# Performance work log

Hardware: AMD Instinct MI355X
Metric: run time of the kernel (lower is better)

## Reference

```python
import jax, jax.numpy as jnp
import numpy as np

B, T, E, H = 512, 256, 384, 64

def setup_inputs() -> dict:
    key = jax.random.key(0)
    k1, k2, k3, k4 = jax.random.split(key, 4)
    scale = 1.0 / np.sqrt(E)
    return {
        "x":  jax.random.normal(k1, (B, T, E), dtype=jnp.float32),
        "Wq": jax.random.normal(k2, (E, H), dtype=jnp.float32) * scale,
        "Wk": jax.random.normal(k3, (E, H), dtype=jnp.float32) * scale,
        "Wv": jax.random.normal(k4, (E, H), dtype=jnp.float32) * scale,
    }

def reference(x, Wq, Wk, Wv):
    # single-head causal self-attention (dropout in eval mode / identity)
    q = jnp.einsum('bte,eh->bth', x, Wq)
    k = jnp.einsum('bte,eh->bth', x, Wk)
    v = jnp.einsum('bte,eh->bth', x, Wv)
    d = q.shape[-1]
    wei = jnp.einsum('bqh,bkh->bqk', q, k) * (d ** -0.5)   # [B,T,T]
    T_ = x.shape[1]
    causal = jnp.tril(jnp.ones((T_, T_), dtype=bool))
    wei = jnp.where(causal[None, :, :], wei, -jnp.inf)
    wei = jax.nn.softmax(wei, axis=-1)
    out = jnp.einsum('bqk,bkh->bqh', wei, v)               # [B,T,H]
    return out
```

## Files before the change

kernel.cpp:

```cpp
#include <hip/hip_runtime.h>

typedef __attribute__((ext_vector_type(4)))  float f32x4;
typedef __attribute__((ext_vector_type(16))) float f32x16;
typedef __attribute__((ext_vector_type(8)))  short s16x8;
typedef __attribute__((ext_vector_type(4)))  short s16x4;


__device__ inline short f2bf(float f){
  unsigned u = __float_as_uint(f);
  u = u + 0x7fffu + ((u >> 16) & 1u);
  return (short)(u >> 16);
}

__device__ __forceinline__ void gld16(const void* g, void* l){
  __builtin_amdgcn_global_load_lds((const __attribute__((address_space(1))) void*)g,
                                   (__attribute__((address_space(3))) void*)l, 16, 0, 0);
}

__global__ void wt_prep_kernel(const float* __restrict__ Wq, const float* __restrict__ Wk,
                               const float* __restrict__ Wv, short* __restrict__ Wt){
  int o = blockIdx.x * 256 + threadIdx.x;
  if (o >= 192*384) return;
  int n = o / 384, k = o - n*384;
  const float* W = (n < 64) ? Wq : (n < 128) ? Wk : Wv;
  Wt[o] = f2bf(W[k*64 + (n & 63)]);
}

__global__ __launch_bounds__(512, 4) void qkv_kernel(const float* __restrict__ x,
    const short* __restrict__ Wt, short* __restrict__ Qg,
    short* __restrict__ Kg, short* __restrict__ Vg){
  const int tid  = threadIdx.x;
  const int w    = tid >> 6, lane = tid & 63;
  const int l15  = lane & 15, quad = lane >> 4;
  const int b    = blockIdx.x;

  const float* xb = x + (long)b*256*384;
  short* Qb = Qg + (long)b*16384;
  char*  Kb = (char*)(Kg + (long)b*16384);
  char*  Vb = (char*)(Vg + (long)b*16384);

  #pragma unroll 1
  for (int p = 0; p < 2; ++p){
    const int r0 = w*32 + p*16;
    const int tr = r0 + l15;

    f32x4 aq[4], ak[4], av[4];
    #pragma unroll
    for (int c = 0; c < 4; ++c)
      #pragma unroll
      for (int i = 0; i < 4; ++i){ aq[c][i]=0.f; ak[c][i]=0.f; av[c][i]=0.f; }

    const float* xr = xb + (long)tr*384;
    #pragma unroll 2
    for (int kt = 0; kt < 12; ++kt){
      const int k0 = kt*32 + quad*8;
      float4 a0 = *(const float4*)(xr + k0);
      float4 a1 = *(const float4*)(xr + k0 + 4);
      s16x8 bx;
      bx[0]=f2bf(a0.x); bx[1]=f2bf(a0.y); bx[2]=f2bf(a0.z); bx[3]=f2bf(a0.w);
      bx[4]=f2bf(a1.x); bx[5]=f2bf(a1.y); bx[6]=f2bf(a1.z); bx[7]=f2bf(a1.w);
      #pragma unroll
      for (int c = 0; c < 4; ++c){
        s16x8 wq = *(const s16x8*)(Wt + (c*16 + l15)*384 + k0);
        aq[c] = __builtin_amdgcn_mfma_f32_16x16x32_bf16(wq, bx, aq[c], 0, 0, 0);
      }
      #pragma unroll
      for (int c = 0; c < 4; ++c){
        s16x8 wk = *(const s16x8*)(Wt + ((c+4)*16 + l15)*384 + k0);
        ak[c] = __builtin_amdgcn_mfma_f32_16x16x32_bf16(wk, bx, ak[c], 0, 0, 0);
      }
      #pragma unroll
      for (int c = 0; c < 4; ++c){
        s16x8 wv = *(const s16x8*)(Wt + ((c+8)*16 + l15)*384 + k0);
        av[c] = __builtin_amdgcn_mfma_f32_16x16x32_bf16(bx, wv, av[c], 0, 0, 0);
      }
    }

    #pragma unroll
    for (int c = 0; c < 4; ++c){
      s16x4 v;
      #pragma unroll
      for (int i = 0; i < 4; ++i) v[i] = f2bf(aq[c][i]);
      *(s16x4*)(Qb + tr*64 + c*16 + quad*4) = v;
    }
    {
      const int swz = (tr & 7) << 4;
      #pragma unroll
      for (int c = 0; c < 4; ++c){
        s16x4 v;
        #pragma unroll
        for (int i = 0; i < 4; ++i) v[i] = f2bf(ak[c][i]);
        *(s16x4*)(Kb + tr*128 + ((c*32 + quad*8) ^ swz)) = v;
      }
    }
    #pragma unroll
    for (int c = 0; c < 4; ++c){
      const int h   = c*16 + l15;
      const int swz = (h & 7) << 4;
      s16x4 v;
      #pragma unroll
      for (int i = 0; i < 4; ++i) v[i] = f2bf(av[c][i]);
      *(s16x4*)(Vb + h*512 + (((r0 + quad*4)*2) ^ swz)) = v;
    }
  }
}

__global__ __launch_bounds__(512, 4) void attn_kernel(const short* __restrict__ Qg,
    const short* __restrict__ Kg, const short* __restrict__ Vg,
    float* __restrict__ out){
  __shared__ __align__(16) short Ks[16384];
  __shared__ __align__(16) short Vts[16384];
  __shared__ __align__(16) short Pp[8][16*40];

  const int tid  = threadIdx.x;
  const int w    = tid >> 6, lane = tid & 63;
  const int l15  = lane & 15, quad = lane >> 4;
  const int b    = blockIdx.x;

  const short* Qb = Qg + (long)b*16384;
  const int F0 = w, F1 = 15 - w;
  s16x8 qA0 = *(const s16x8*)(Qb + (F0*16 + l15)*64 + quad*8);
  s16x8 qA1 = *(const s16x8*)(Qb + (F0*16 + l15)*64 + 32 + quad*8);
  s16x8 qB0 = *(const s16x8*)(Qb + (F1*16 + l15)*64 + quad*8);
  s16x8 qB1 = *(const s16x8*)(Qb + (F1*16 + l15)*64 + 32 + quad*8);

  const char* Kb = (const char*)(Kg + (long)b*16384);
  const char* Vb = (const char*)(Vg + (long)b*16384);
  {
    const int base = w*4096;
    #pragma unroll
    for (int i = 0; i < 4; ++i){
      gld16(Kb + base + i*1024 + lane*16, (char*)Ks  + base + i*1024);
      gld16(Vb + base + i*1024 + lane*16, (char*)Vts + base + i*1024);
    }
  }
  __syncthreads();

  float* ob = out + (long)b*256*64;
  short* Pw = Pp[w];
  const int swz = (l15 & 7) << 4;

  auto attend = [&](int F, s16x8 qf0, s16x8 qf1){
    const int qb = F*16;
    const int NF = F + 1;
    const int NS = (NF + 1) >> 1;

    f32x4 sc[16];
    #pragma unroll
    for (int f = 0; f < 16; ++f){
      f32x4 a;
      #pragma unroll
      for (int r = 0; r < 4; ++r) a[r] = 0.0f;
      if (f < NF){
        const char* kp = (const char*)Ks + (f*16 + l15)*128;
        s16x8 k0v = *(const s16x8*)(kp + ((quad*16)      ^ swz));
        s16x8 k1v = *(const s16x8*)(kp + ((64 + quad*16) ^ swz));
        a = __builtin_amdgcn_mfma_f32_16x16x32_bf16(qf0, k0v, a, 0, 0, 0);
        a = __builtin_amdgcn_mfma_f32_16x16x32_bf16(qf1, k1v, a, 0, 0, 0);
      }
      sc[f] = a;
    }

    float mx[4], sm[4];
    #pragma unroll
    for (int r = 0; r < 4; ++r) mx[r] = -3.0e38f;
    #pragma unroll
    for (int f = 0; f < 16; ++f){
      if (f < NF){
        const int key = f*16 + l15;
        #pragma unroll
        for (int r = 0; r < 4; ++r){
          const int qg = qb + quad*4 + r;
          float s = sc[f][r] * 0.125f;
          s = (key <= qg) ? s : -1.0e30f;
          sc[f][r] = s;
          mx[r] = fmaxf(mx[r], s);
        }
      }
    }
    #pragma unroll
    for (int r = 0; r < 4; ++r){
      #pragma unroll
      for (int off = 1; off < 16; off <<= 1) mx[r] = fmaxf(mx[r], __shfl_xor(mx[r], off, 16));
    }
    #pragma unroll
    for (int r = 0; r < 4; ++r) sm[r] = 0.0f;
    #pragma unroll
    for (int f = 0; f < 16; ++f){
      if (f < NF){
        #pragma unroll
        for (int r = 0; r < 4; ++r){
          float p = exp2f((sc[f][r] - mx[r]) * 1.44269504f);
          sc[f][r] = p;
          sm[r] += p;
        }
      }
    }
    #pragma unroll
    for (int r = 0; r < 4; ++r){
      #pragma unroll
      for (int off = 1; off < 16; off <<= 1) sm[r] += __shfl_xor(sm[r], off, 16);
    }

    f32x4 o[4];
    #pragma unroll
    for (int h0 = 0; h0 < 4; ++h0)
      #pragma unroll
      for (int r = 0; r < 4; ++r) o[h0][r] = 0.0f;

    #pragma unroll
    for (int ks = 0; ks < 8; ++ks){
      if (ks < NS){
        #pragma unroll
        for (int fi = 0; fi < 2; ++fi){
          const int f = 2*ks + fi;
          #pragma unroll
          for (int r = 0; r < 4; ++r){
            short v = 0;
            if (f < NF) v = f2bf(sc[f][r]);
            Pw[(quad*4 + r)*40 + fi*16 + l15] = v;
          }
        }
        s16x8 pf = *(const s16x8*)(Pw + l15*40 + quad*8);
        #pragma unroll
        for (int h0 = 0; h0 < 4; ++h0){
          const char* vp = (const char*)Vts + (h0*16 + l15)*512;
          s16x8 vf = *(const s16x8*)(vp + ((ks*64 + quad*16) ^ swz));
          o[h0] = __builtin_amdgcn_mfma_f32_16x16x32_bf16(pf, vf, o[h0], 0, 0, 0);
        }
      }
    }

    #pragma unroll
    for (int r = 0; r < 4; ++r){
      const float inv = 1.0f / sm[r];
      #pragma unroll
      for (int h0 = 0; h0 < 4; ++h0)
        ob[(qb + quad*4 + r)*64 + h0*16 + l15] = o[h0][r] * inv;
    }
  };
  attend(F0, qA0, qA1);
  attend(F1, qB0, qB1);
}

__global__ __launch_bounds__(512, 2) void fused_kernel(const float* __restrict__ x,
                             const short* __restrict__ Wt, float* __restrict__ out){
  __shared__ __align__(16) short Qs[256*72];
  __shared__ __align__(16) short Ks2[256*72];
  __shared__ __align__(16) short Vts2[64*264];
  __shared__ __align__(16) short Pp2[8][16*40];

  const int tid  = threadIdx.x;
  const int w    = tid >> 6, lane = tid & 63;
  const int l31  = lane & 31, hh = lane >> 5;
  const int b    = blockIdx.x;

  const float* xb = x + ((long)b*256 + w*32)*384;

  f32x16 acc[6];
  #pragma unroll
  for (int c = 0; c < 6; ++c)
    #pragma unroll
    for (int j = 0; j < 16; ++j) acc[c][j] = 0.0f;

  #pragma unroll 2
  for (int kt = 0; kt < 6; ++kt){
    #pragma unroll
    for (int s = 0; s < 4; ++s){
      const int k0 = kt*64 + s*16 + hh*8;
      const float* xp = xb + l31*384 + k0;
      float4 a0 = *(const float4*)xp;
      float4 a1 = *(const float4*)(xp + 4);
      s16x8 bx;
      bx[0]=f2bf(a0.x); bx[1]=f2bf(a0.y); bx[2]=f2bf(a0.z); bx[3]=f2bf(a0.w);
      bx[4]=f2bf(a1.x); bx[5]=f2bf(a1.y); bx[6]=f2bf(a1.z); bx[7]=f2bf(a1.w);
      #pragma unroll
      for (int c = 0; c < 6; ++c){
        s16x8 wa = *(const s16x8*)(Wt + (c*32 + l31)*384 + k0);
        acc[c] = __builtin_amdgcn_mfma_f32_32x32x16_bf16(wa, bx, acc[c], 0, 0, 0);
      }
    }
  }

  const int trow = w*32 + l31;
  #pragma unroll
  for (int c = 0; c < 4; ++c){
    short* dst = (c < 2) ? Qs : Ks2;
    const int nb = (c & 1)*32;
    #pragma unroll
    for (int g = 0; g < 4; ++g){
      s16x4 v;
      #pragma unroll
      for (int i = 0; i < 4; ++i) v[i] = f2bf(acc[c][g*4 + i]);
      *(s16x4*)(dst + trow*72 + nb + 8*g + 4*hh) = v;
    }
  }
  #pragma unroll
  for (int c = 4; c < 6; ++c)
    #pragma unroll
    for (int reg = 0; reg < 16; ++reg){
      const int h = (c-4)*32 + (reg & 3) + 8*(reg >> 2) + 4*hh;
      Vts2[h*264 + trow] = f2bf(acc[c][reg]);
    }

  __syncthreads();

  const int l15 = lane & 15, quad = lane >> 4;
  float* ob = out + (long)b*256*64;
  short* Pw = Pp2[w];

  for (int it = 0; it < 2; ++it){
    const int F  = it ? (15 - w) : w;
    const int qb = F*16;
    const int NF = F + 1;
    const int NS = (NF + 1) >> 1;

    s16x8 qf0 = *(const s16x8*)(Qs + (qb + l15)*72 + quad*8);
    s16x8 qf1 = *(const s16x8*)(Qs + (qb + l15)*72 + 32 + quad*8);

    f32x4 sc[16];
    #pragma unroll
    for (int f = 0; f < 16; ++f){
      f32x4 a;
      #pragma unroll
      for (int r = 0; r < 4; ++r) a[r] = 0.0f;
      if (f < NF){
        const short* kp = Ks2 + (f*16 + l15)*72 + quad*8;
        s16x8 k0v = *(const s16x8*)kp;
        s16x8 k1v = *(const s16x8*)(kp + 32);
        a = __builtin_amdgcn_mfma_f32_16x16x32_bf16(qf0, k0v, a, 0, 0, 0);
        a = __builtin_amdgcn_mfma_f32_16x16x32_bf16(qf1, k1v, a, 0, 0, 0);
      }
      sc[f] = a;
    }

    float mx[4], sm[4];
    #pragma unroll
    for (int r = 0; r < 4; ++r) mx[r] = -3.0e38f;
    #pragma unroll
    for (int f = 0; f < 16; ++f){
      if (f < NF){
        const int key = f*16 + l15;
        #pragma unroll
        for (int r = 0; r < 4; ++r){
          const int qg = qb + quad*4 + r;
          float s = sc[f][r] * 0.125f;
          s = (key <= qg) ? s : -1.0e30f;
          sc[f][r] = s;
          mx[r] = fmaxf(mx[r], s);
        }
      }
    }
    #pragma unroll
    for (int r = 0; r < 4; ++r){
      #pragma unroll
      for (int off = 1; off < 16; off <<= 1) mx[r] = fmaxf(mx[r], __shfl_xor(mx[r], off, 16));
    }
    #pragma unroll
    for (int r = 0; r < 4; ++r) sm[r] = 0.0f;
    #pragma unroll
    for (int f = 0; f < 16; ++f){
      if (f < NF){
        #pragma unroll
        for (int r = 0; r < 4; ++r){
          float p = exp2f((sc[f][r] - mx[r]) * 1.44269504f);
          sc[f][r] = p;
          sm[r] += p;
        }
      }
    }
    #pragma unroll
    for (int r = 0; r < 4; ++r){
      #pragma unroll
      for (int off = 1; off < 16; off <<= 1) sm[r] += __shfl_xor(sm[r], off, 16);
    }

    f32x4 o[4];
    #pragma unroll
    for (int h0 = 0; h0 < 4; ++h0)
      #pragma unroll
      for (int r = 0; r < 4; ++r) o[h0][r] = 0.0f;

    #pragma unroll
    for (int ks = 0; ks < 8; ++ks){
      if (ks < NS){
        #pragma unroll
        for (int fi = 0; fi < 2; ++fi){
          const int f = 2*ks + fi;
          #pragma unroll
          for (int r = 0; r < 4; ++r){
            short v = 0;
            if (f < NF) v = f2bf(sc[f][r]);
            Pw[(quad*4 + r)*40 + fi*16 + l15] = v;
          }
        }
        s16x8 pf = *(const s16x8*)(Pw + l15*40 + quad*8);
        #pragma unroll
        for (int h0 = 0; h0 < 4; ++h0){
          s16x8 vf = *(const s16x8*)(Vts2 + (h0*16 + l15)*264 + ks*32 + quad*8);
          o[h0] = __builtin_amdgcn_mfma_f32_16x16x32_bf16(pf, vf, o[h0], 0, 0, 0);
        }
      }
    }

    #pragma unroll
    for (int r = 0; r < 4; ++r){
      const float inv = 1.0f / sm[r];
      #pragma unroll
      for (int h0 = 0; h0 < 4; ++h0)
        ob[(qb + quad*4 + r)*64 + h0*16 + l15] = o[h0][r] * inv;
    }
  }
}

extern "C" void kernel_launch(void* const* d_in, const int* in_sizes, int n_in,
                              void* d_out, int out_size, void* d_ws, size_t ws_size,
                              hipStream_t stream){
  const float* x  = (const float*)d_in[0];
  const float* Wq = (const float*)d_in[1];
  const float* Wk = (const float*)d_in[2];
  const float* Wv = (const float*)d_in[3];
  float* out = (float*)d_out;

  short* Wt = (short*)d_ws;
  const size_t need = 147456 + 3ull*16777216ull;

  hipLaunchKernelGGL(wt_prep_kernel, dim3(288), dim3(256), 0, stream, Wq, Wk, Wv, Wt);
  if (ws_size >= need){
    short* Qg = (short*)((char*)d_ws + 147456);
    short* Kg = Qg + 8388608;
    short* Vg = Kg + 8388608;
    hipLaunchKernelGGL(qkv_kernel,  dim3(512), dim3(512), 0, stream, x, Wt, Qg, Kg, Vg);
    hipLaunchKernelGGL(attn_kernel, dim3(512), dim3(512), 0, stream, Qg, Kg, Vg, out);
  } else {
    hipLaunchKernelGGL(fused_kernel, dim3(512), dim3(512), 0, stream, x, Wt, out);
  }
}
```

Baseline: 424.1 us.

## Restructure QKV projection with LDS-staged double-buffered x tiles and 32x32 MFMA

The QKV projection kernel now splits each batch across two blocks of 128 rows. It stages x tiles into swizzled LDS with async global-to-LDS loads, double-buffered across the K loop, and computes with 32x32x16 MFMAs split across two warp groups. This targets the strided, uncoalesced per-lane global reads of x and raises parallelism, at the cost of a barrier each K step. The fallback fused kernel is also replaced by one that projects into LDS directly with the attention tiling, but that path likely does not run when the workspace is large enough.

```diff
diff --git a/kernel.cpp b/kernel.cpp
--- a/kernel.cpp
+++ b/kernel.cpp
@@ -26,31 +26,283 @@
   Wt[o] = f2bf(W[k*64 + (n & 63)]);
 }
 
-__global__ __launch_bounds__(512, 4) void qkv_kernel(const float* __restrict__ x,
+__global__ __launch_bounds__(512, 4) void qkv2_kernel(const float* __restrict__ x,
     const short* __restrict__ Wt, short* __restrict__ Qg,
     short* __restrict__ Kg, short* __restrict__ Vg){
+  __shared__ __align__(16) float xs[2][128][32];
+
+  const int tid  = threadIdx.x;
+  const int w    = tid >> 6, lane = tid & 63;
+  const int l31  = lane & 31, hh = lane >> 5;
+  const int wn   = w >> 2,  wt = w & 3;
+  const int b    = blockIdx.x >> 1;
+  const int t0   = (blockIdx.x & 1) << 7;
+
+  const char* xbase = (const char*)x + ((long)b*256 + t0)*1536;
+
+  auto stage = [&](int kt, int buf){
+    #pragma unroll
+    for (int i2 = 0; i2 < 2; ++i2){
+      const int ii = w*2 + i2;
+      const int r  = ii*8 + (lane >> 3);
+      const char* src = xbase + (long)r*1536 + kt*128
+                      + ((((lane & 7) ^ (lane >> 3)) << 4));
+      gld16(src, (char*)&xs[buf][ii*8][0]);
+    }
+  };
+
+  f32x16 acc[3];
+  #pragma unroll
+  for (int c = 0; c < 3; ++c)
+    #pragma unroll
+    for (int i = 0; i < 16; ++i) acc[c][i] = 0.0f;
+
+  const int swr = (l31 & 7) << 4;
+  const short* wrow = Wt + (wn*96 + l31)*384;
+
+  stage(0, 0);
+  __syncthreads();
+
+  for (int kt = 0; kt < 12; ++kt){
+    if (kt < 11) stage(kt + 1, (kt + 1) & 1);
+
+    const char* bp = (const char*)&xs[kt & 1][wt*32 + l31][0];
+    #pragma unroll
+    for (int s = 0; s < 2; ++s){
+      const int c0 = s*64 + hh*32;
+      f32x4 a0 = *(const f32x4*)(bp + ((c0     ) ^ swr));
+      f32x4 a1 = *(const f32x4*)(bp + ((c0 + 16) ^ swr));
+      s16x8 bx;
+      bx[0]=f2bf(a0[0]); bx[1]=f2bf(a0[1]); bx[2]=f2bf(a0[2]); bx[3]=f2bf(a0[3]);
+      bx[4]=f2bf(a1[0]); bx[5]=f2bf(a1[1]); bx[6]=f2bf(a1[2]); bx[7]=f2bf(a1[3]);
+
+      const short* wp = wrow + kt*32 + s*16 + hh*8;
+      s16x8 w0 = *(const s16x8*)(wp);
+      s16x8 w1 = *(const s16x8*)(wp + 32*384);
+      s16x8 w2 = *(const s16x8*)(wp + 64*384);
+      if (wn == 0){
+        acc[0] = __builtin_amdgcn_mfma_f32_32x32x16_bf16(w0, bx, acc[0], 0, 0, 0);
+        acc[1] = __builtin_amdgcn_mfma_f32_32x32x16_bf16(w1, bx, acc[1], 0, 0, 0);
+        acc[2] = __builtin_amdgcn_mfma_f32_32x32x16_bf16(w2, bx, acc[2], 0, 0, 0);
+      } else {
+        acc[0] = __builtin_amdgcn_mfma_f32_32x32x16_bf16(w0, bx, acc[0], 0, 0, 0);
+        acc[1] = __builtin_amdgcn_mfma_f32_32x32x16_bf16(bx, w1, acc[1], 0, 0, 0);
+        acc[2] = __builtin_amdgcn_mfma_f32_32x32x16_bf16(bx, w2, acc[2], 0, 0, 0);
+      }
+    }
+    __syncthreads();
+  }
+
+  const int tl = t0 + wt*32 + l31;
+  short* Qb = Qg + (long)b*16384;
+  char*  Kb = (char*)(Kg + (long)b*16384);
+  char*  Vb = (char*)(Vg + (long)b*16384);
+
+  if (wn == 0){
+    #pragma unroll
+    for (int c = 0; c < 2; ++c)
+      #pragma unroll
+      for (int g = 0; g < 4; ++g){
+        s16x4 v;
+        #pragma unroll
+        for (int j = 0; j < 4; ++j) v[j] = f2bf(acc[c][4*g + j]);
+        *(s16x4*)(Qb + (long)tl*64 + c*32 + 8*g + 4*hh) = v;
+      }
+    const int swk = (tl & 7) << 4;
+    #pragma unroll
+    for (int g = 0; g < 4; ++g){
+      s16x4 v;
+      #pragma unroll
+      for (int j = 0; j < 4; ++j) v[j] = f2bf(acc[2][4*g + j]);
+      *(s16x4*)(Kb + (long)tl*128 + ((16*g + 8*hh) ^ swk)) = v;
+    }
+  } else {
+    const int swk = (tl & 7) << 4;
+    #pragma unroll
+    for (int g = 0; g < 4; ++g){
+      s16x4 v;
+      #pragma unroll
+      for (int j = 0; j < 4; ++j) v[j] = f2bf(acc[0][4*g + j]);
+      *(s16x4*)(Kb + (long)tl*128 + ((64 + 16*g + 8*hh) ^ swk)) = v;
+    }
+    #pragma unroll
+    for (int c = 1; c < 3; ++c){
+      const int h   = (c - 1)*32 + l31;
+      const int swv = (h & 7) << 4;
+      #pragma unroll
+      for (int g = 0; g < 4; ++g){
+        const int tb = t0 + wt*32 + 8*g + 4*hh;
+        s16x4 v;
+        #pragma unroll
+        for (int j = 0; j < 4; ++j) v[j] = f2bf(acc[c][4*g + j]);
+        *(s16x4*)(Vb + (long)h*512 + ((tb*2) ^ swv)) = v;
+      }
+    }
+  }
+}
+
+__global__ __launch_bounds__(512, 4) void attn_kernel(const short* __restrict__ Qg,
+    const short* __restrict__ Kg, const short* __restrict__ Vg,
+    float* __restrict__ out){
+  __shared__ __align__(16) short Ks[16384];
+  __shared__ __align__(16) short Vts[16384];
+  __shared__ __align__(16) short Pp[8][16*40];
+
   const int tid  = threadIdx.x;
   const int w    = tid >> 6, lane = tid & 63;
   const int l15  = lane & 15, quad = lane >> 4;
   const int b    = blockIdx.x;
 
+  const short* Qb = Qg + (long)b*16384;
+  const int F0 = w, F1 = 15 - w;
+  s16x8 qA0 = *(const s16x8*)(Qb + (F0*16 + l15)*64 + quad*8);
+  s16x8 qA1 = *(const s16x8*)(Qb + (F0*16 + l15)*64 + 32 + quad*8);
+  s16x8 qB0 = *(const s16x8*)(Qb + (F1*16 + l15)*64 + quad*8);
+  s16x8 qB1 = *(const s16x8*)(Qb + (F1*16 + l15)*64 + 32 + quad*8);
+
+  const char* Kb = (const char*)(Kg + (long)b*16384);
+  const char* Vb = (const char*)(Vg + (long)b*16384);
+  {
+    const int base = w*4096;
+    #pragma unroll
+    for (int i = 0; i < 4; ++i){
+      gld16(Kb + base + i*1024 + lane*16, (char*)Ks  + base + i*1024);
+      gld16(Vb + base + i*1024 + lane*16, (char*)Vts + base + i*1024);
+    }
+  }
+  __syncthreads();
+
+  float* ob = out + (long)b*256*64;
+  short* Pw = Pp[w];
+  const int swz = (l15 & 7) << 4;
+
+  auto attend = [&](int F, s16x8 qf0, s16x8 qf1){
+    const int qb = F*16;
+    const int NF = F + 1;
+    const int NS = (NF + 1) >> 1;
+
+    f32x4 sc[16];
+    #pragma unroll
+    for (int f = 0; f < 16; ++f){
+      f32x4 a;
+      #pragma unroll
+      for (int r = 0; r < 4; ++r) a[r] = 0.0f;
+      if (f < NF){
+        const char* kp = (const char*)Ks + (f*16 + l15)*128;
+        s16x8 k0v = *(const s16x8*)(kp + ((quad*16)      ^ swz));
+        s16x8 k1v = *(const s16x8*)(kp + ((64 + quad*16) ^ swz));
+        a = __builtin_amdgcn_mfma_f32_16x16x32_bf16(qf0, k0v, a, 0, 0, 0);
+        a = __builtin_amdgcn_mfma_f32_16x16x32_bf16(qf1, k1v, a, 0, 0, 0);
+      }
+      sc[f] = a;
+    }
+
+    float mx[4], sm[4];
+    #pragma unroll
+    for (int r = 0; r < 4; ++r) mx[r] = -3.0e38f;
+    #pragma unroll
+    for (int f = 0; f < 16; ++f){
+      if (f < NF){
+        const int key = f*16 + l15;
+        #pragma unroll
+        for (int r = 0; r < 4; ++r){
+          const int qg = qb + quad*4 + r;
+          float s = sc[f][r] * 0.125f;
+          s = (key <= qg) ? s : -1.0e30f;
+          sc[f][r] = s;
+          mx[r] = fmaxf(mx[r], s);
+        }
+      }
+    }
+    #pragma unroll
+    for (int r = 0; r < 4; ++r){
+      #pragma unroll
+      for (int off = 1; off < 16; off <<= 1) mx[r] = fmaxf(mx[r], __shfl_xor(mx[r], off, 16));
+    }
+    #pragma unroll
+    for (int r = 0; r < 4; ++r) sm[r] = 0.0f;
+    #pragma unroll
+    for (int f = 0; f < 16; ++f){
+      if (f < NF){
+        #pragma unroll
+        for (int r = 0; r < 4; ++r){
+          float p = exp2f((sc[f][r] - mx[r]) * 1.44269504f);
+          sc[f][r] = p;
+          sm[r] += p;
+        }
+      }
+    }
+    #pragma unroll
+    for (int r = 0; r < 4; ++r){
+      #pragma unroll
+      for (int off = 1; off < 16; off <<= 1) sm[r] += __shfl_xor(sm[r], off, 16);
+    }
+
+    f32x4 o[4];
+    #pragma unroll
+    for (int h0 = 0; h0 < 4; ++h0)
+      #pragma unroll
+      for (int r = 0; r < 4; ++r) o[h0][r] = 0.0f;
+
+    #pragma unroll
+    for (int ks = 0; ks < 8; ++ks){
+      if (ks < NS){
+        #pragma unroll
+        for (int fi = 0; fi < 2; ++fi){
+          const int f = 2*ks + fi;
+          #pragma unroll
+          for (int r = 0; r < 4; ++r){
+            short v = 0;
+            if (f < NF) v = f2bf(sc[f][r]);
+            Pw[(quad*4 + r)*40 + fi*16 + l15] = v;
+          }
+        }
+        s16x8 pf = *(const s16x8*)(Pw + l15*40 + quad*8);
+        #pragma unroll
+        for (int h0 = 0; h0 < 4; ++h0){
+          const char* vp = (const char*)Vts + (h0*16 + l15)*512;
+          s16x8 vf = *(const s16x8*)(vp + ((ks*64 + quad*16) ^ swz));
+          o[h0] = __builtin_amdgcn_mfma_f32_16x16x32_bf16(pf, vf, o[h0], 0, 0, 0);
+        }
+      }
+    }
+
+    #pragma unroll
+    for (int r = 0; r < 4; ++r){
+      const float inv = 1.0f / sm[r];
+      #pragma unroll
+      for (int h0 = 0; h0 < 4; ++h0)
+        ob[(qb + quad*4 + r)*64 + h0*16 + l15] = o[h0][r] * inv;
+    }
+  };
+  attend(F0, qA0, qA1);
+  attend(F1, qB0, qB1);
+}
+
+__global__ __launch_bounds__(512, 4) void fused2_kernel(const float* __restrict__ x,
+                             const short* __restrict__ Wt, float* __restrict__ out){
+  __shared__ __align__(16) char  KsB[32768];
+  __shared__ __align__(16) char  VtsB[32768];
+  __shared__ __align__(16) short Pp[8][16*40];
+
+  const int tid  = threadIdx.x;
+  const int w    = tid >> 6, lane = tid & 63;
+  const int l15  = lane & 15, quad = lane >> 4;
+  const int b    = blockIdx.x;
+
   const float* xb = x + (long)b*256*384;
-  short* Qb = Qg + (long)b*16384;
-  char*  Kb = (char*)(Kg + (long)b*16384);
-  char*  Vb = (char*)(Vg + (long)b*16384);
-
-  #pragma unroll 1
-  for (int p = 0; p < 2; ++p){
-    const int r0 = w*32 + p*16;
-    const int tr = r0 + l15;
-
+  const int F0 = w, F1 = 15 - w;
+
+  s16x8 qA0, qA1, qB0, qB1;
+
+  auto project = [&](int r0, s16x8& qf0, s16x8& qf1){
     f32x4 aq[4], ak[4], av[4];
     #pragma unroll
     for (int c = 0; c < 4; ++c)
       #pragma unroll
       for (int i = 0; i < 4; ++i){ aq[c][i]=0.f; ak[c][i]=0.f; av[c][i]=0.f; }
 
-    const float* xr = xb + (long)tr*384;
+    const float* xr = xb + (long)(r0 + l15)*384;
     #pragma unroll 2
     for (int kt = 0; kt < 12; ++kt){
       const int k0 = kt*32 + quad*8;
@@ -76,64 +328,41 @@
       }
     }
 
+    char* krow = KsB + (r0 + l15)*128;
+    const int swzr = (l15 & 7) << 4;
+
     #pragma unroll
     for (int c = 0; c < 4; ++c){
       s16x4 v;
       #pragma unroll
       for (int i = 0; i < 4; ++i) v[i] = f2bf(aq[c][i]);
-      *(s16x4*)(Qb + tr*64 + c*16 + quad*4) = v;
-    }
-    {
-      const int swz = (tr & 7) << 4;
-      #pragma unroll
-      for (int c = 0; c < 4; ++c){
-        s16x4 v;
-        #pragma unroll
-        for (int i = 0; i < 4; ++i) v[i] = f2bf(ak[c][i]);
-        *(s16x4*)(Kb + tr*128 + ((c*32 + quad*8) ^ swz)) = v;
-      }
-    }
+      *(s16x4*)(krow + ((c*32 + quad*8) ^ swzr)) = v;
+    }
+    asm volatile("s_waitcnt lgkmcnt(0)" ::: "memory");
+    qf0 = *(const s16x8*)(krow + ((quad*16)      ^ swzr));
+    qf1 = *(const s16x8*)(krow + ((64 + quad*16) ^ swzr));
+    asm volatile("s_waitcnt lgkmcnt(0)" ::: "memory");
+
     #pragma unroll
     for (int c = 0; c < 4; ++c){
-      const int h   = c*16 + l15;
-      const int swz = (h & 7) << 4;
       s16x4 v;
       #pragma unroll
+      for (int i = 0; i < 4; ++i) v[i] = f2bf(ak[c][i]);
+      *(s16x4*)(krow + ((c*32 + quad*8) ^ swzr)) = v;
+    }
+    #pragma unroll
+    for (int c = 0; c < 4; ++c){
+      const int h = c*16 + l15;
+      s16x4 v;
+      #pragma unroll
       for (int i = 0; i < 4; ++i) v[i] = f2bf(av[c][i]);
-      *(s16x4*)(Vb + h*512 + (((r0 + quad*4)*2) ^ swz)) = v;
-    }
-  }
-}
-
-__global__ __launch_bounds__(512, 4) void attn_kernel(const short* __restrict__ Qg,
-    const short* __restrict__ Kg, const short* __restrict__ Vg,
-    float* __restrict__ out){
-  __shared__ __align__(16) short Ks[16384];
-  __shared__ __align__(16) short Vts[16384];
-  __shared__ __align__(16) short Pp[8][16*40];
-
-  const int tid  = threadIdx.x;
-  const int w    = tid >> 6, lane = tid & 63;
-  const int l15  = lane & 15, quad = lane >> 4;
-  const int b    = blockIdx.x;
-
-  const short* Qb = Qg + (long)b*16384;
-  const int F0 = w, F1 = 15 - w;
-  s16x8 qA0 = *(const s16x8*)(Qb + (F0*16 + l15)*64 + quad*8);
-  s16x8 qA1 = *(const s16x8*)(Qb + (F0*16 + l15)*64 + 32 + quad*8);
-  s16x8 qB0 = *(const s16x8*)(Qb + (F1*16 + l15)*64 + quad*8);
-  s16x8 qB1 = *(const s16x8*)(Qb + (F1*16 + l15)*64 + 32 + quad*8);
-
-  const char* Kb = (const char*)(Kg + (long)b*16384);
-  const char* Vb = (const char*)(Vg + (long)b*16384);
-  {
-    const int base = w*4096;
-    #pragma unroll
-    for (int i = 0; i < 4; ++i){
-      gld16(Kb + base + i*1024 + lane*16, (char*)Ks  + base + i*1024);
-      gld16(Vb + base + i*1024 + lane*16, (char*)Vts + base + i*1024);
-    }
-  }
+      *(s16x4*)(VtsB + h*512 + (((r0 + quad*4)*2) ^ ((h & 7) << 4))) = v;
+    }
+  };
+
+  project(F0*16, qA0, qA1);
+  project(F1*16, qB0, qB1);
+
   __syncthreads();
 
   float* ob = out + (long)b*256*64;
@@ -152,7 +381,7 @@
       #pragma unroll
       for (int r = 0; r < 4; ++r) a[r] = 0.0f;
       if (f < NF){
-        const char* kp = (const char*)Ks + (f*16 + l15)*128;
+        const char* kp = KsB + (f*16 + l15)*128;
         s16x8 k0v = *(const s16x8*)(kp + ((quad*16)      ^ swz));
         s16x8 k1v = *(const s16x8*)(kp + ((64 + quad*16) ^ swz));
         a = __builtin_amdgcn_mfma_f32_16x16x32_bf16(qf0, k0v, a, 0, 0, 0);
@@ -224,7 +453,7 @@
         s16x8 pf = *(const s16x8*)(Pw + l15*40 + quad*8);
         #pragma unroll
         for (int h0 = 0; h0 < 4; ++h0){
-          const char* vp = (const char*)Vts + (h0*16 + l15)*512;
+          const char* vp = VtsB + (h0*16 + l15)*512;
           s16x8 vf = *(const s16x8*)(vp + ((ks*64 + quad*16) ^ swz));
           o[h0] = __builtin_amdgcn_mfma_f32_16x16x32_bf16(pf, vf, o[h0], 0, 0, 0);
         }
@@ -239,178 +468,9 @@
         ob[(qb + quad*4 + r)*64 + h0*16 + l15] = o[h0][r] * inv;
     }
   };
+
   attend(F0, qA0, qA1);
   attend(F1, qB0, qB1);
-}
-
-__global__ __launch_bounds__(512, 2) void fused_kernel(const float* __restrict__ x,
-                             const short* __restrict__ Wt, float* __restrict__ out){
-  __shared__ __align__(16) short Qs[256*72];
-  __shared__ __align__(16) short Ks2[256*72];
-  __shared__ __align__(16) short Vts2[64*264];
-  __shared__ __align__(16) short Pp2[8][16*40];
-
-  const int tid  = threadIdx.x;
-  const int w    = tid >> 6, lane = tid & 63;
-  const int l31  = lane & 31, hh = lane >> 5;
-  const int b    = blockIdx.x;
-
-  const float* xb = x + ((long)b*256 + w*32)*384;
-
-  f32x16 acc[6];
-  #pragma unroll
-  for (int c = 0; c < 6; ++c)
-    #pragma unroll
-    for (int j = 0; j < 16; ++j) acc[c][j] = 0.0f;
-
-  #pragma unroll 2
-  for (int kt = 0; kt < 6; ++kt){
-    #pragma unroll
-    for (int s = 0; s < 4; ++s){
-      const int k0 = kt*64 + s*16 + hh*8;
-      const float* xp = xb + l31*384 + k0;
-      float4 a0 = *(const float4*)xp;
-      float4 a1 = *(const float4*)(xp + 4);
-      s16x8 bx;
-      bx[0]=f2bf(a0.x); bx[1]=f2bf(a0.y); bx[2]=f2bf(a0.z); bx[3]=f2bf(a0.w);
-      bx[4]=f2bf(a1.x); bx[5]=f2bf(a1.y); bx[6]=f2bf(a1.z); bx[7]=f2bf(a1.w);
-      #pragma unroll
-      for (int c = 0; c < 6; ++c){
-        s16x8 wa = *(const s16x8*)(Wt + (c*32 + l31)*384 + k0);
-        acc[c] = __builtin_amdgcn_mfma_f32_32x32x16_bf16(wa, bx, acc[c], 0, 0, 0);
-      }
-    }
-  }
-
-  const int trow = w*32 + l31;
-  #pragma unroll
-  for (int c = 0; c < 4; ++c){
-    short* dst = (c < 2) ? Qs : Ks2;
-    const int nb = (c & 1)*32;
-    #pragma unroll
-    for (int g = 0; g < 4; ++g){
-      s16x4 v;
-      #pragma unroll
-      for (int i = 0; i < 4; ++i) v[i] = f2bf(acc[c][g*4 + i]);
-      *(s16x4*)(dst + trow*72 + nb + 8*g + 4*hh) = v;
-    }
-  }
-  #pragma unroll
-  for (int c = 4; c < 6; ++c)
-    #pragma unroll
-    for (int reg = 0; reg < 16; ++reg){
-      const int h = (c-4)*32 + (reg & 3) + 8*(reg >> 2) + 4*hh;
-      Vts2[h*264 + trow] = f2bf(acc[c][reg]);
-    }
-
-  __syncthreads();
-
-  const int l15 = lane & 15, quad = lane >> 4;
-  float* ob = out + (long)b*256*64;
-  short* Pw = Pp2[w];
-
-  for (int it = 0; it < 2; ++it){
-    const int F  = it ? (15 - w) : w;
-    const int qb = F*16;
-    const int NF = F + 1;
-    const int NS = (NF + 1) >> 1;
-
-    s16x8 qf0 = *(const s16x8*)(Qs + (qb + l15)*72 + quad*8);
-    s16x8 qf1 = *(const s16x8*)(Qs + (qb + l15)*72 + 32 + quad*8);
-
-    f32x4 sc[16];
-    #pragma unroll
-    for (int f = 0; f < 16; ++f){
-      f32x4 a;
-      #pragma unroll
-      for (int r = 0; r < 4; ++r) a[r] = 0.0f;
-      if (f < NF){
-        const short* kp = Ks2 + (f*16 + l15)*72 + quad*8;
-        s16x8 k0v = *(const s16x8*)kp;
-        s16x8 k1v = *(const s16x8*)(kp + 32);
-        a = __builtin_amdgcn_mfma_f32_16x16x32_bf16(qf0, k0v, a, 0, 0, 0);
-        a = __builtin_amdgcn_mfma_f32_16x16x32_bf16(qf1, k1v, a, 0, 0, 0);
-      }
-      sc[f] = a;
-    }
-
-    float mx[4], sm[4];
-    #pragma unroll
-    for (int r = 0; r < 4; ++r) mx[r] = -3.0e38f;
-    #pragma unroll
-    for (int f = 0; f < 16; ++f){
-      if (f < NF){
-        const int key = f*16 + l15;
-        #pragma unroll
-        for (int r = 0; r < 4; ++r){
-          const int qg = qb + quad*4 + r;
-          float s = sc[f][r] * 0.125f;
-          s = (key <= qg) ? s : -1.0e30f;
-          sc[f][r] = s;
-          mx[r] = fmaxf(mx[r], s);
-        }
-      }
-    }
-    #pragma unroll
-    for (int r = 0; r < 4; ++r){
-      #pragma unroll
-      for (int off = 1; off < 16; off <<= 1) mx[r] = fmaxf(mx[r], __shfl_xor(mx[r], off, 16));
-    }
-    #pragma unroll
-    for (int r = 0; r < 4; ++r) sm[r] = 0.0f;
-    #pragma unroll
-    for (int f = 0; f < 16; ++f){
-      if (f < NF){
-        #pragma unroll
-        for (int r = 0; r < 4; ++r){
-          float p = exp2f((sc[f][r] - mx[r]) * 1.44269504f);
-          sc[f][r] = p;
-          sm[r] += p;
-        }
-      }
-    }
-    #pragma unroll
-    for (int r = 0; r < 4; ++r){
-      #pragma unroll
-      for (int off = 1; off < 16; off <<= 1) sm[r] += __shfl_xor(sm[r], off, 16);
-    }
-
-    f32x4 o[4];
-    #pragma unroll
-    for (int h0 = 0; h0 < 4; ++h0)
-      #pragma unroll
-      for (int r = 0; r < 4; ++r) o[h0][r] = 0.0f;
-
-    #pragma unroll
-    for (int ks = 0; ks < 8; ++ks){
-      if (ks < NS){
-        #pragma unroll
-        for (int fi = 0; fi < 2; ++fi){
-          const int f = 2*ks + fi;
-          #pragma unroll
-          for (int r = 0; r < 4; ++r){
-            short v = 0;
-            if (f < NF) v = f2bf(sc[f][r]);
-            Pw[(quad*4 + r)*40 + fi*16 + l15] = v;
-          }
-        }
-        s16x8 pf = *(const s16x8*)(Pw + l15*40 + quad*8);
-        #pragma unroll
-        for (int h0 = 0; h0 < 4; ++h0){
-          s16x8 vf = *(const s16x8*)(Vts2 + (h0*16 + l15)*264 + ks*32 + quad*8);
-          o[h0] = __builtin_amdgcn_mfma_f32_16x16x32_bf16(pf, vf, o[h0], 0, 0, 0);
-        }
-      }
-    }
-
-    #pragma unroll
-    for (int r = 0; r < 4; ++r){
-      const float inv = 1.0f / sm[r];
-      #pragma unroll
-      for (int h0 = 0; h0 < 4; ++h0)
-        ob[(qb + quad*4 + r)*64 + h0*16 + l15] = o[h0][r] * inv;
-    }
-  }
 }
 
 extern "C" void kernel_launch(void* const* d_in, const int* in_sizes, int n_in,
@@ -430,9 +490,9 @@
     short* Qg = (short*)((char*)d_ws + 147456);
     short* Kg = Qg + 8388608;
     short* Vg = Kg + 8388608;
-    hipLaunchKernelGGL(qkv_kernel,  dim3(512), dim3(512), 0, stream, x, Wt, Qg, Kg, Vg);
-    hipLaunchKernelGGL(attn_kernel, dim3(512), dim3(512), 0, stream, Qg, Kg, Vg, out);
+    hipLaunchKernelGGL(qkv2_kernel, dim3(1024), dim3(512), 0, stream, x, Wt, Qg, Kg, Vg);
+    hipLaunchKernelGGL(attn_kernel, dim3(512),  dim3(512), 0, stream, Qg, Kg, Vg, out);
   } else {
-    hipLaunchKernelGGL(fused_kernel, dim3(512), dim3(512), 0, stream, x, Wt, out);
+    hipLaunchKernelGGL(fused2_kernel, dim3(512), dim3(512), 0, stream, x, Wt, out);
   }
 }
```

New measurement: 364.2 us. 14.1% less time.
